# Kernel optimization log

Hardware: AMD Instinct MI355X
Metric: run time of the kernel (lower is better)

Reference implementation:

```python
import jax, jax.numpy as jnp
import numpy as np

B_, H_, W_, DM = 32, 64, 64, 256
D_INNER, D_STATE, NHEADS, HEADDIM = 512, 64, 8, 64
D_IN_PROJ = D_INNER + 2 * D_STATE + NHEADS  # 648


def setup_inputs() -> dict:
    key = jax.random.key(0)
    ks = jax.random.split(key, 4)
    x = jax.random.normal(ks[0], (B_, H_, W_, DM), dtype=jnp.float32)
    W_in = jax.random.normal(ks[1], (DM, D_IN_PROJ), dtype=jnp.float32) * 0.05
    dt_bias = jax.random.normal(ks[2], (NHEADS,), dtype=jnp.float32)
    A_log = jax.random.uniform(ks[3], (NHEADS,), dtype=jnp.float32)  # A in [1, e)
    D_param = jnp.ones((NHEADS,), dtype=jnp.float32)
    ln_gamma = jnp.ones((D_INNER,), dtype=jnp.float32)
    ln_beta = jnp.zeros((D_INNER,), dtype=jnp.float32)
    W_out = jax.random.normal(jax.random.fold_in(key, 7), (D_INNER, DM), dtype=jnp.float32) * 0.05
    return {"x": x, "W_in": W_in, "dt_bias": dt_bias, "A_log": A_log,
            "D_param": D_param, "ln_gamma": ln_gamma, "ln_beta": ln_beta, "W_out": W_out}


def reference(x, W_in, dt_bias, A_log, D_param, ln_gamma, ln_beta, W_out):
    B, H, W, Dm = x.shape
    L = H * W
    u = x.reshape(B, L, Dm)
    A = -jnp.exp(A_log)  # (nheads,), negative
    xbcdt = u @ W_in  # (B, L, 648)
    x_ssm = xbcdt[..., :D_INNER]                          # (B, L, d_inner)
    B_ssm = xbcdt[..., D_INNER:D_INNER + D_STATE]         # (B, L, d_state) ~ K
    C_ssm = xbcdt[..., D_INNER + D_STATE:D_INNER + 2 * D_STATE]  # (B, L, d_state) ~ Q
    dt = jax.nn.softplus(xbcdt[..., D_INNER + 2 * D_STATE:] + dt_bias)  # (B, L, nheads)
    V = x_ssm.reshape(B, L, NHEADS, HEADDIM)  # (B, L, h, p)
    # dA gating: dt * A per head (defaults: no exp/softmax/norm variants)
    dA = dt * A  # (B, L, h)
    V_scaled = V * dA[..., None]  # (B, L, h, p)
    # linear-attention dual: KV = K^T @ V_scaled, then Q @ KV
    KV = jnp.einsum('bls,blhp->bhsp', B_ssm, V_scaled)  # (B, h, d_state, p)
    y = jnp.einsum('bls,bhsp->blhp', C_ssm, KV)         # (B, L, h, p)
    # D skip (per-head)
    y = y + V * D_param[None, None, :, None]
    y = y.reshape(B, L, D_INNER)
    # LayerNorm
    mu = jnp.mean(y, axis=-1, keepdims=True)
    var = jnp.var(y, axis=-1, keepdims=True)
    y = (y - mu) / jnp.sqrt(var + 1e-5) * ln_gamma + ln_beta
    out = y @ W_out
    return out.reshape(B, H, W, Dm)
```

## Files before the change

### kernel.cpp

```cpp
#include <hip/hip_runtime.h>
#include <hip/hip_bf16.h>
#include <math.h>

constexpr int B_N   = 32;
constexpr int L_N   = 4096;
constexpr int DM    = 256;
constexpr int DIN   = 512;
constexpr int DS    = 64;
constexpr int NH    = 8;
constexpr int HD    = 64;
constexpr int M_N   = B_N * L_N;
constexpr int XBW   = 640;
constexpr int YST   = 536;
constexpr int AST   = 268;

typedef unsigned short u16;
typedef short s16x4 __attribute__((ext_vector_type(4)));
typedef short s16x8 __attribute__((ext_vector_type(8)));
typedef float f32x4 __attribute__((ext_vector_type(4)));
typedef unsigned short u16x8 __attribute__((ext_vector_type(8)));
typedef unsigned short u16x4 __attribute__((ext_vector_type(4)));

__device__ __forceinline__ float softplusf(float z) {
  return (z > 20.f) ? z : log1pf(expf(z));
}
__device__ __forceinline__ u16 f2bf(float f) {
  unsigned u = __float_as_uint(f);
  u += 0x7FFFu + ((u >> 16) & 1u);
  return (u16)(u >> 16);
}
__device__ __forceinline__ float bf2f(u16 u) {
  return __uint_as_float(((unsigned)u) << 16);
}
__device__ __forceinline__ s16x8 ld_frag2(const short* p) {
  s16x4 lo = *(const s16x4*)p;
  s16x4 hi = *(const s16x4*)(p + 4);
  s16x8 r;
  r[0]=lo[0]; r[1]=lo[1]; r[2]=lo[2]; r[3]=lo[3];
  r[4]=hi[0]; r[5]=hi[1]; r[6]=hi[2]; r[7]=hi[3];
  return r;
}

#define GLDS(gsrc, ldst)                                                       \
  __builtin_amdgcn_global_load_lds(                                            \
      (const __attribute__((address_space(1))) void*)(gsrc),                   \
      (__attribute__((address_space(3))) void*)(ldst), 16, 0, 0)

constexpr long CW1 = 768L * 256;
constexpr long CW2 = CW1 + 256L * 512;
__global__ __launch_bounds__(256) void k_cvt(
    const float* __restrict__ Wi, const float* __restrict__ Wo,
    u16* __restrict__ WinT, u16* __restrict__ WoT) {
  for (long i = (long)blockIdx.x * 256 + threadIdx.x; i < CW2;
       i += (long)gridDim.x * 256) {
    if (i < CW1) {
      int n = (int)(i >> 8); int k = (int)(i & 255);
      WinT[i] = (n < 648) ? f2bf(Wi[(size_t)k * 648 + n]) : (u16)0;
    } else {
      long t = i - CW1; int n = (int)(t >> 9); int k = (int)(t & 511);
      WoT[t] = f2bf(Wo[(size_t)k * 256 + n]);
    }
  }
}

__global__ __launch_bounds__(256) void k_inproj(
    const float* __restrict__ x, const u16* __restrict__ WinT,
    const float* __restrict__ dt_bias, const float* __restrict__ A_log,
    u16* __restrict__ xbcdt, float* __restrict__ dAv) {
  __shared__ __align__(16) short sA[128 * AST];
  __shared__ __align__(16) short sB[128 * 32];
  const int tid = threadIdx.x;
  const int wave = tid >> 6, lane = tid & 63;
  const int m0 = blockIdx.x * 128;
  const int wr = wave >> 1, wc = wave & 1;
  const int fr = lane & 15, fq = lane >> 4;

#pragma unroll
  for (int q = 0; q < 32; ++q) {
    int idx = tid + q * 256;
    int row = idx >> 6, c4 = idx & 63;
    float4 v = *(const float4*)(x + (size_t)(m0 + row) * DM + c4 * 4);
    u16x4 o = {f2bf(v.x), f2bf(v.y), f2bf(v.z), f2bf(v.w)};
    *(u16x4*)&sA[row * AST + c4 * 4] = o;
  }
  __syncthreads();

  int rowB[2], kcB[2], ldsOffB[2];
#pragma unroll
  for (int q = 0; q < 2; ++q) {
    int G = wave * 128 + q * 64 + lane;
    rowB[q] = G >> 2; kcB[q] = G & 3;
    ldsOffB[q] = G * 8;
  }

  for (int nt = 0; nt < 6; ++nt) {
    const int n0 = nt * 128;
    f32x4 acc[4][4] = {};
    for (int k0 = 0; k0 < DM; k0 += 32) {
      if (nt || k0) __syncthreads();
#pragma unroll
      for (int q = 0; q < 2; ++q)
        GLDS(WinT + (size_t)(n0 + rowB[q]) * DM + kcB[q] * 8 + k0, sB + ldsOffB[q]);
      __syncthreads();
      const int kb = fq * 8;
      s16x8 af[4], bf[4];
#pragma unroll
      for (int i = 0; i < 4; ++i)
        af[i] = ld_frag2(&sA[(wr * 64 + i * 16 + fr) * AST + k0 + kb]);
#pragma unroll
      for (int j = 0; j < 4; ++j)
        bf[j] = *(const s16x8*)&sB[(wc * 64 + j * 16 + fr) * 32 + kb];
#pragma unroll
      for (int i = 0; i < 4; ++i)
#pragma unroll
        for (int j = 0; j < 4; ++j)
          acc[i][j] = __builtin_amdgcn_mfma_f32_16x16x32_bf16(af[i], bf[j], acc[i][j], 0, 0, 0);
    }
    const int row_base = m0 + wr * 64 + fq * 4;
    if (n0 < 640) {
      const int col_base = n0 + wc * 64;
#pragma unroll
      for (int i = 0; i < 4; ++i)
#pragma unroll
        for (int r = 0; r < 4; ++r) {
          int row = row_base + i * 16 + r;
#pragma unroll
          for (int j = 0; j < 4; ++j)
            xbcdt[(size_t)row * XBW + col_base + j * 16 + fr] = f2bf(acc[i][j][r]);
        }
    } else if (wc == 0 && fr < 8) {
      const float nAe = -expf(A_log[fr]);
      const float db = dt_bias[fr];
#pragma unroll
      for (int i = 0; i < 4; ++i)
#pragma unroll
        for (int r = 0; r < 4; ++r) {
          int row = row_base + i * 16 + r;
          dAv[(size_t)row * NH + fr] = softplusf(acc[i][0][r] + db) * nAe;
        }
    }
  }
}

__global__ __launch_bounds__(256) void k_bt(
    const u16* __restrict__ xbcdt, u16* __restrict__ Bt) {
  __shared__ u16 sT[64][72];
  const int m0 = blockIdx.x * 64;
  const int b  = m0 >> 12;
  const int l0 = m0 & (L_N - 1);
  const int tid = threadIdx.x;
#pragma unroll
  for (int q = 0; q < 2; ++q) {
    int r = (tid >> 3) + q * 32, c8 = (tid & 7) * 8;
    u16x8 v = *(const u16x8*)&xbcdt[(size_t)(m0 + r) * XBW + DIN + c8];
#pragma unroll
    for (int jj = 0; jj < 8; ++jj) sT[r][c8 + jj] = v[jj];
  }
  __syncthreads();
#pragma unroll
  for (int q = 0; q < 2; ++q) {
    int s = (tid >> 3) + q * 32, lc8 = (tid & 7) * 8;
    u16x8 o;
#pragma unroll
    for (int jj = 0; jj < 8; ++jj) o[jj] = sT[lc8 + jj][s];
    *(u16x8*)&Bt[((size_t)(b * 64 + s)) * L_N + l0 + lc8] = o;
  }
}

__global__ __launch_bounds__(256) void k_kv(
    const u16* __restrict__ xbcdt, const u16* __restrict__ Bt,
    const float* __restrict__ dAv, float* __restrict__ KVp) {
  const int bh = blockIdx.y;
  const int b = bh >> 3, h = bh & 7;
  const int l0 = blockIdx.x * (L_N / 4);
  const int tid = threadIdx.x;
  const int wave = tid >> 6, lane = tid & 63;
  const int wr = wave >> 1, wc = wave & 1;
  const int fr = lane & 15, fq = lane >> 4;
  __shared__ short sBt[64 * 36];
  __shared__ short sVt[64 * 36];
  f32x4 acc[2][2] = {};
  const int ts = tid >> 2, tlc = tid & 3;
  const int tl = tid >> 3, tpg = tid & 7;

  for (int ks = 0; ks < L_N / 4; ks += 32) {
    u16x8 vb = *(const u16x8*)&Bt[((size_t)(b * 64 + ts)) * L_N + l0 + ks + tlc * 8];
    const int gl = b * L_N + l0 + ks + tl;
    u16x8 vv = *(const u16x8*)&xbcdt[(size_t)gl * XBW + h * HD + tpg * 8];
    const float da = dAv[(size_t)gl * NH + h];
    __syncthreads();
    *(s16x4*)&sBt[ts * 36 + tlc * 8]     = *(s16x4*)&vb;
    *(s16x4*)&sBt[ts * 36 + tlc * 8 + 4] = *((s16x4*)&vb + 1);
#pragma unroll
    for (int jj = 0; jj < 8; ++jj)
      sVt[(tpg * 8 + jj) * 36 + tl] = (short)f2bf(bf2f(vv[jj]) * da);
    __syncthreads();
    s16x8 af[2], bf[2];
#pragma unroll
    for (int i = 0; i < 2; ++i)
      af[i] = ld_frag2(&sBt[(wr * 32 + i * 16 + fr) * 36 + fq * 8]);
#pragma unroll
    for (int j = 0; j < 2; ++j)
      bf[j] = ld_frag2(&sVt[(wc * 32 + j * 16 + fr) * 36 + fq * 8]);
#pragma unroll
    for (int i = 0; i < 2; ++i)
#pragma unroll
      for (int j = 0; j < 2; ++j)
        acc[i][j] = __builtin_amdgcn_mfma_f32_16x16x32_bf16(af[i], bf[j], acc[i][j], 0, 0, 0);
  }
  float* dst = KVp + ((size_t)(blockIdx.x * 256 + bh)) * 4096;
#pragma unroll
  for (int i = 0; i < 2; ++i)
#pragma unroll
    for (int j = 0; j < 2; ++j) {
      int p = wc * 32 + j * 16 + fr;
      int s0 = wr * 32 + i * 16 + fq * 4;
      float4 v;
      v.x = acc[i][j][0]; v.y = acc[i][j][1];
      v.z = acc[i][j][2]; v.w = acc[i][j][3];
      *(float4*)&dst[p * 64 + s0] = v;
    }
}

__global__ __launch_bounds__(256) void k_kvsum(
    const float* __restrict__ KVp, u16* __restrict__ KVt) {
  const int bh = blockIdx.x;
  const int tid = threadIdx.x;
  const float* src = KVp + (size_t)bh * 4096;
#pragma unroll
  for (int q = 0; q < 4; ++q) {
    int i4 = (tid + q * 256) * 4;
    float4 v0 = *(const float4*)(src + i4);
    float4 v1 = *(const float4*)(src + 1048576 + i4);
    float4 v2 = *(const float4*)(src + 2097152 + i4);
    float4 v3 = *(const float4*)(src + 3145728 + i4);
    u16x4 o = {f2bf(v0.x + v1.x + v2.x + v3.x),
               f2bf(v0.y + v1.y + v2.y + v3.y),
               f2bf(v0.z + v1.z + v2.z + v3.z),
               f2bf(v0.w + v1.w + v2.w + v3.w)};
    *(u16x4*)&KVt[(size_t)bh * 4096 + i4] = o;
  }
}

__global__ __launch_bounds__(256) void k_fused(
    const u16* __restrict__ xb, const u16* __restrict__ KVt,
    const float* __restrict__ Dp, const float* __restrict__ g,
    const float* __restrict__ bt, const u16* __restrict__ WoT,
    float* __restrict__ out) {
  __shared__ __align__(16) short sC[64 * 76];
  __shared__ __align__(16) short sY[64 * YST];
  const int tid = threadIdx.x;
  const int wave = tid >> 6, lane = tid & 63;
  const int fr = lane & 15, fq = lane >> 4;
  const int m0 = blockIdx.x * 64;
  const int b = m0 >> 12;

#pragma unroll
  for (int q = 0; q < 2; ++q) {
    int idx = tid + q * 256;
    int row = idx >> 3, c8 = (idx & 7) * 8;
    u16x8 v = *(const u16x8*)&xb[(size_t)(m0 + row) * XBW + DIN + DS + c8];
    *(u16x8*)&sC[row * 76 + c8] = v;
  }
  __syncthreads();

#pragma unroll
  for (int hh = 0; hh < 2; ++hh) {
    const int h = wave + hh * 4;
    const u16* kt = KVt + (size_t)(b * NH + h) * 4096;
    f32x4 acc[4][4] = {};
#pragma unroll
    for (int kk = 0; kk < 2; ++kk) {
      s16x8 af[4], bf[4];
#pragma unroll
      for (int i = 0; i < 4; ++i)
        af[i] = *(const s16x8*)&sC[(i * 16 + fr) * 76 + kk * 32 + fq * 8];
#pragma unroll
      for (int j = 0; j < 4; ++j)
        bf[j] = *(const s16x8*)&kt[(j * 16 + fr) * 64 + kk * 32 + fq * 8];
#pragma unroll
      for (int i = 0; i < 4; ++i)
#pragma unroll
        for (int j = 0; j < 4; ++j)
          acc[i][j] = __builtin_amdgcn_mfma_f32_16x16x32_bf16(af[i], bf[j], acc[i][j], 0, 0, 0);
    }
#pragma unroll
    for (int i = 0; i < 4; ++i)
#pragma unroll
      for (int r = 0; r < 4; ++r) {
        int rl = i * 16 + fq * 4 + r;
#pragma unroll
        for (int j = 0; j < 4; ++j)
          sY[rl * YST + h * HD + j * 16 + fr] = (short)f2bf(acc[i][j][r]);
      }
  }
  __syncthreads();

  {
    const int row = tid >> 2, seg4 = tid & 3;
    const u16* vrow = xb + (size_t)(m0 + row) * XBW;
    float s = 0.f, q = 0.f;
#pragma unroll
    for (int c = 0; c < 16; ++c) {
      int k0 = seg4 * 8 + c * 32;
      const float ds = Dp[c >> 1];
      u16x8 v = *(const u16x8*)&sY[row * YST + k0];
      u16x8 w = *(const u16x8*)(vrow + k0);
      u16x8 o;
#pragma unroll
      for (int jj = 0; jj < 8; ++jj) {
        float f = bf2f(v[jj]) + ds * bf2f(w[jj]);
        s += f; q += f * f;
        o[jj] = f2bf(f);
      }
      *(u16x8*)&sY[row * YST + k0] = o;
    }
    s += __shfl_xor(s, 1); q += __shfl_xor(q, 1);
    s += __shfl_xor(s, 2); q += __shfl_xor(q, 2);
    const float mu = s / DIN;
    const float rstd = rsqrtf(q / DIN - mu * mu + 1e-5f);
#pragma unroll
    for (int c = 0; c < 16; ++c) {
      int k0 = seg4 * 8 + c * 32;
      u16x8 v = *(const u16x8*)&sY[row * YST + k0];
      float4 g0 = *(const float4*)(g + k0);
      float4 g1 = *(const float4*)(g + k0 + 4);
      float4 b0 = *(const float4*)(bt + k0);
      float4 b1 = *(const float4*)(bt + k0 + 4);
      u16x8 o;
      o[0] = f2bf((bf2f(v[0]) - mu) * rstd * g0.x + b0.x);
      o[1] = f2bf((bf2f(v[1]) - mu) * rstd * g0.y + b0.y);
      o[2] = f2bf((bf2f(v[2]) - mu) * rstd * g0.z + b0.z);
      o[3] = f2bf((bf2f(v[3]) - mu) * rstd * g0.w + b0.w);
      o[4] = f2bf((bf2f(v[4]) - mu) * rstd * g1.x + b1.x);
      o[5] = f2bf((bf2f(v[5]) - mu) * rstd * g1.y + b1.y);
      o[6] = f2bf((bf2f(v[6]) - mu) * rstd * g1.z + b1.z);
      o[7] = f2bf((bf2f(v[7]) - mu) * rstd * g1.w + b1.w);
      *(u16x8*)&sY[row * YST + k0] = o;
    }
  }
  __syncthreads();

  {
    f32x4 acc2[4][4] = {};
#pragma unroll
    for (int kk = 0; kk < 16; ++kk) {
      s16x8 af2[4], bf2[4];
#pragma unroll
      for (int i = 0; i < 4; ++i)
        af2[i] = *(const s16x8*)&sY[(i * 16 + fr) * YST + kk * 32 + fq * 8];
#pragma unroll
      for (int j = 0; j < 4; ++j)
        bf2[j] = *(const s16x8*)&WoT[(size_t)(wave * 64 + j * 16 + fr) * DIN + kk * 32 + fq * 8];
#pragma unroll
      for (int i = 0; i < 4; ++i)
#pragma unroll
        for (int j = 0; j < 4; ++j)
          acc2[i][j] = __builtin_amdgcn_mfma_f32_16x16x32_bf16(af2[i], bf2[j], acc2[i][j], 0, 0, 0);
    }
#pragma unroll
    for (int i = 0; i < 4; ++i)
#pragma unroll
      for (int r = 0; r < 4; ++r) {
        int row = m0 + i * 16 + fq * 4 + r;
#pragma unroll
        for (int j = 0; j < 4; ++j)
          out[(size_t)row * DM + wave * 64 + j * 16 + fr] = acc2[i][j][r];
      }
  }
}

extern "C" void kernel_launch(void* const* d_in, const int* in_sizes, int n_in,
                              void* d_out, int out_size, void* d_ws, size_t ws_size,
                              hipStream_t stream) {
  const float* x       = (const float*)d_in[0];
  const float* W_in    = (const float*)d_in[1];
  const float* dt_bias = (const float*)d_in[2];
  const float* A_log   = (const float*)d_in[3];
  const float* D_param = (const float*)d_in[4];
  const float* gamma   = (const float*)d_in[5];
  const float* beta    = (const float*)d_in[6];
  const float* W_out   = (const float*)d_in[7];
  float* out = (float*)d_out;

  u16* ws    = (u16*)d_ws;
  u16* WinT  = ws;
  u16* WoT   = WinT + 768L * 256;
  u16* xbcdt = WoT + 256L * 512;
  u16* Bt    = xbcdt + (size_t)M_N * XBW;
  float* dAv = (float*)(Bt + (size_t)B_N * 64 * L_N);
  float* KVp = dAv + (size_t)M_N * NH;
  u16* KVt   = (u16*)(KVp + 4L * 256 * 4096);

  k_cvt    <<<256, 256, 0, stream>>>(W_in, W_out, WinT, WoT);
  k_inproj <<<M_N / 128, 256, 0, stream>>>(x, WinT, dt_bias, A_log, xbcdt, dAv);
  k_bt     <<<M_N / 64, 256, 0, stream>>>(xbcdt, Bt);
  k_kv     <<<dim3(4, B_N * NH), 256, 0, stream>>>(xbcdt, Bt, dAv, KVp);
  k_kvsum  <<<B_N * NH, 256, 0, stream>>>(KVp, KVt);
  k_fused  <<<M_N / 64, 256, 0, stream>>>(xbcdt, KVt, D_param, gamma, beta, WoT, out);
}
```

Before: 285.1 us.

## Swap MFMA operands, prefetch KV fragments, and vectorize transposed Y stores

The Q·KV epilogue GEMM now uses the KV tile as the A operand and C as the B operand. The output comes out transposed, so each lane holds four consecutive columns and can store them as one 8-byte vector write to shared memory instead of scalar stores. The first head's KV fragments are loaded before the barrier, and the second head's are issued while the first head's MFMAs run, which hides global load latency. C fragments are loaded once and reused for both heads, at the cost of more registers held live.

New measurement: 283.9 us. About the same (-0.4%).

```diff
diff --git a/kernel.cpp b/kernel.cpp
--- a/kernel.cpp
+++ b/kernel.cpp
@@ -262,37 +262,52 @@
     u16x8 v = *(const u16x8*)&xb[(size_t)(m0 + row) * XBW + DIN + DS + c8];
     *(u16x8*)&sC[row * 76 + c8] = v;
   }
-  __syncthreads();
-
-#pragma unroll
-  for (int hh = 0; hh < 2; ++hh) {
-    const int h = wave + hh * 4;
-    const u16* kt = KVt + (size_t)(b * NH + h) * 4096;
-    f32x4 acc[4][4] = {};
-#pragma unroll
-    for (int kk = 0; kk < 2; ++kk) {
-      s16x8 af[4], bf[4];
-#pragma unroll
-      for (int i = 0; i < 4; ++i)
-        af[i] = *(const s16x8*)&sC[(i * 16 + fr) * 76 + kk * 32 + fq * 8];
+
+  {
+    s16x8 ktf[2][4];
+    const u16* kt0 = KVt + (size_t)(b * NH + wave) * 4096;
+#pragma unroll
+    for (int kk = 0; kk < 2; ++kk)
+#pragma unroll
+      for (int i = 0; i < 4; ++i)
+        ktf[kk][i] = *(const s16x8*)&kt0[(i * 16 + fr) * 64 + kk * 32 + fq * 8];
+    __syncthreads();
+
+    s16x8 cf[2][4];
+#pragma unroll
+    for (int kk = 0; kk < 2; ++kk)
 #pragma unroll
       for (int j = 0; j < 4; ++j)
-        bf[j] = *(const s16x8*)&kt[(j * 16 + fr) * 64 + kk * 32 + fq * 8];
-#pragma unroll
-      for (int i = 0; i < 4; ++i)
-#pragma unroll
-        for (int j = 0; j < 4; ++j)
-          acc[i][j] = __builtin_amdgcn_mfma_f32_16x16x32_bf16(af[i], bf[j], acc[i][j], 0, 0, 0);
-    }
-#pragma unroll
-    for (int i = 0; i < 4; ++i)
-#pragma unroll
-      for (int r = 0; r < 4; ++r) {
-        int rl = i * 16 + fq * 4 + r;
-#pragma unroll
-        for (int j = 0; j < 4; ++j)
-          sY[rl * YST + h * HD + j * 16 + fr] = (short)f2bf(acc[i][j][r]);
+        cf[kk][j] = *(const s16x8*)&sC[(j * 16 + fr) * 76 + kk * 32 + fq * 8];
+
+#pragma unroll
+    for (int hh = 0; hh < 2; ++hh) {
+      const int h = wave + hh * 4;
+      f32x4 acc[4][4] = {};
+#pragma unroll
+      for (int kk = 0; kk < 2; ++kk)
+#pragma unroll
+        for (int i = 0; i < 4; ++i)
+#pragma unroll
+          for (int j = 0; j < 4; ++j)
+            acc[i][j] = __builtin_amdgcn_mfma_f32_16x16x32_bf16(ktf[kk][i], cf[kk][j], acc[i][j], 0, 0, 0);
+      if (hh == 0) {
+        const u16* kt1 = KVt + (size_t)(b * NH + wave + 4) * 4096;
+#pragma unroll
+        for (int kk = 0; kk < 2; ++kk)
+#pragma unroll
+          for (int i = 0; i < 4; ++i)
+            ktf[kk][i] = *(const s16x8*)&kt1[(i * 16 + fr) * 64 + kk * 32 + fq * 8];
       }
+#pragma unroll
+      for (int i = 0; i < 4; ++i)
+#pragma unroll
+        for (int j = 0; j < 4; ++j) {
+          u16x4 o = {f2bf(acc[i][j][0]), f2bf(acc[i][j][1]),
+                     f2bf(acc[i][j][2]), f2bf(acc[i][j][3])};
+          *(u16x4*)&sY[(j * 16 + fr) * YST + h * 64 + i * 16 + fq * 4] = o;
+        }
+    }
   }
   __syncthreads();
 
```
